# Kernel tuning notes

Measured on AMD Instinct MI355X. Metric: run time of the kernel, lower is better.

Reference implementation:

```python
import jax, jax.numpy as jnp
import numpy as np
import math

D_MODEL, N_HEADS, BATCH, SEQ = 1024, 16, 2, 2048
D_HEAD = D_MODEL // N_HEADS


def setup_inputs() -> dict:
    key = jax.random.key(0)
    ks = jax.random.split(key, 5)
    w = lambda k: jax.random.normal(k, (D_MODEL, D_MODEL), jnp.float32) * 0.02
    return {
        "X": jax.random.normal(ks[0], (BATCH, SEQ, D_MODEL), jnp.float32),
        "W_q": w(ks[1]),
        "W_k": w(ks[2]),
        "W_v": w(ks[3]),
        "W_o": w(ks[4]),
        "g_q": jnp.ones((D_MODEL,), jnp.float32),
        "b_q": jnp.zeros((D_MODEL,), jnp.float32),
        "g_k": jnp.ones((D_MODEL,), jnp.float32),
        "b_k": jnp.zeros((D_MODEL,), jnp.float32),
        "cache_k": jnp.zeros((BATCH, N_HEADS, SEQ, D_HEAD), jnp.float32),
        "cache_v": jnp.zeros((BATCH, N_HEADS, SEQ, D_HEAD), jnp.float32),
        "start_pos": 0,
    }


def _layernorm(x, g, b, eps=1e-5):
    mu = jnp.mean(x, axis=-1, keepdims=True)
    xc = x - mu
    var = jnp.mean(xc * xc, axis=-1, keepdims=True)
    return xc * jax.lax.rsqrt(var + eps) * g + b


def reference(X, W_q, W_k, W_v, W_o, g_q, b_q, g_k, b_k, cache_k, cache_v, start_pos):
    batch, N, d_model = X.shape
    H = cache_k.shape[1]
    dh = d_model // H

    # QK-normed projections (torch Linear: x @ W^T)
    XQ = _layernorm(X @ W_q.T, g_q, b_q)
    XK = _layernorm(X @ W_k.T, g_k, b_k)
    XV = X @ W_v.T
    split = lambda t: t.reshape(batch, N, H, dh).transpose(0, 2, 1, 3)  # [b,h,n,d]
    XQ, XK, XV = split(XQ), split(XK), split(XV)

    # KV-cache scatter update, then slice to valid prefix (start_pos is static)
    cache_k = jax.lax.dynamic_update_slice(cache_k, XK, (0, 0, start_pos, 0))
    cache_v = jax.lax.dynamic_update_slice(cache_v, XV, (0, 0, start_pos, 0))
    M = start_pos + N
    K = cache_k[:, :, :M]
    V = cache_v[:, :, :M]

    logits = jnp.einsum('bhnd,bhmd->bhnm', XQ, K) / math.sqrt(dh)  # [b,h,N,M]

    # causal mask on the freshly written block [start_pos:M]
    tril = jnp.tril(jnp.ones((N, N), bool))
    full_mask = jnp.concatenate([jnp.ones((N, start_pos), bool), tril], axis=1)  # [N,M]
    logits = jnp.where(full_mask[None, None], logits, -jnp.inf)

    # selective forget-mask bias built from relu'd head-0 logits
    S = jax.nn.relu(logits[:, 0])               # relu(-inf) -> 0, matches torch
    S = S.at[..., 0].set(0.0)                   # zero first column
    S = S * (1.0 - jnp.eye(N, dtype=S.dtype))   # zero diagonal (valid since start_pos==0)
    S = jnp.roll(S, 1, axis=-2)                 # shift rows down by one
    S = S.at[..., 0, :].set(0.0)
    F_mask = jnp.cumsum(S, axis=-2)             # [b,N,M]

    logits = logits - F_mask[:, None]
    attn = jax.nn.softmax(logits, axis=-1)
    O = jnp.einsum('bhnm,bhmd->bhnd', attn, V)
    O = O.transpose(0, 2, 1, 3).reshape(batch, N, d_model)
    return O @ W_o.T
```

## Files before the change

kernel.cpp:

```cpp
#include <hip/hip_runtime.h>
#include <cstdint>
#include <cstddef>


typedef unsigned short u16;
typedef __attribute__((ext_vector_type(8))) __bf16 bf16x8;
typedef __attribute__((ext_vector_type(4))) float f32x4;

#define D_MODEL 1024
#define N_HEADS 16
#define BATCH   2
#define SEQ     2048
#define D_HEAD  64
#define ROWS    (BATCH*SEQ)
#define NSEG    16
#define SEGLEN  128
#define LOG2E   1.44269504f

static __device__ __forceinline__ u16 f2bf(float f){
  union { float f; uint32_t u; } v; v.f = f;
  uint32_t r = v.u + 0x7fffu + ((v.u >> 16) & 1u);
  return (u16)(r >> 16);
}
static __device__ __forceinline__ float bf2f(u16 h){
  union { uint32_t u; float f; } v; v.u = ((uint32_t)h) << 16;
  return v.f;
}
static __device__ __forceinline__ uint32_t pack2(float a, float b){
  uint32_t ua = __float_as_uint(a) + 0x8000u;
  uint32_t ub = __float_as_uint(b) + 0x8000u;
  return (ua >> 16) | (ub & 0xffff0000u);
}

__global__ void k_cast_split_all(const float* __restrict__ X,
                                 u16* __restrict__ Xhi, u16* __restrict__ Xlo,
                                 const float* __restrict__ Wq,
                                 u16* __restrict__ Wqh, u16* __restrict__ Wql,
                                 const float* __restrict__ Wk,
                                 u16* __restrict__ Wkh, u16* __restrict__ Wkl){
  int i = blockIdx.x*256 + threadIdx.x;
  const float* src; u16 *dh, *dl; int base;
  if (i < 1048576){ src = X;  dh = Xhi; dl = Xlo; base = i; }
  else if (i < 1310720){ src = Wq; dh = Wqh; dl = Wql; base = i - 1048576; }
  else { src = Wk; dh = Wkh; dl = Wkl; base = i - 1310720; }
  float4 v = reinterpret_cast<const float4*>(src)[base];
  float vs[4] = {v.x, v.y, v.z, v.w};
  union { u16 s[4]; uint2 u; } uh, ul;
#pragma unroll
  for (int r=0;r<4;++r){
    uh.s[r] = f2bf(vs[r]);
    ul.s[r] = f2bf(vs[r] - bf2f(uh.s[r]));
  }
  reinterpret_cast<uint2*>(dh)[base] = uh.u;
  reinterpret_cast<uint2*>(dl)[base] = ul.u;
}

__global__ void k_cast2(const float* __restrict__ Wv, u16* __restrict__ Wvb,
                        const float* __restrict__ Wo, u16* __restrict__ Wob){
  int i = blockIdx.x*256 + threadIdx.x;
  const float* src; u16* dst; int base;
  if (i < 262144){ src = Wv; dst = Wvb; base = i; }
  else { src = Wo; dst = Wob; base = i - 262144; }
  float4 v = reinterpret_cast<const float4*>(src)[base];
  float vs[4] = {v.x, v.y, v.z, v.w};
  union { u16 s[4]; uint2 u; } uh;
#pragma unroll
  for (int r=0;r<4;++r) uh.s[r] = f2bf(vs[r]);
  reinterpret_cast<uint2*>(dst)[base] = uh.u;
}

__global__ __launch_bounds__(256) void k_gemm_qk(
    const u16* __restrict__ Xhi, const u16* __restrict__ Xlo,
    const u16* __restrict__ Wh, const u16* __restrict__ Wl,
    float* __restrict__ C)
{
  __shared__ __align__(16) u16 As[128*32];
  __shared__ __align__(16) u16 Bs[128*32];
  const int tid = threadIdx.x, wv = tid>>6, ln = tid&63;
  const int lane15 = ln&15, quad = ln>>4;
  const int wm = wv&1, wn = wv>>1;
  const size_t rowBase = (size_t)blockIdx.y*128, colBase = (size_t)blockIdx.x*128;
  const int npass = ((blockIdx.x & 7) == 0) ? 3 : 1;
  f32x4 acc[4][4];
  f32x4 z = {0.f,0.f,0.f,0.f};
#pragma unroll
  for (int i=0;i<4;++i)
#pragma unroll
    for (int j=0;j<4;++j) acc[i][j] = z;
  const u16* Aps[3] = {Xhi, Xhi, Xlo};
  const u16* Bps[3] = {Wh, Wl, Wh};
  const int sRow = ln>>2, sCol = (ln&3)*8;
  for (int p = 0; p < npass; ++p) {
    const u16* Ap = Aps[p];
    const u16* Bp = Bps[p];
    for (int kt = 0; kt < 32; ++kt) {
      __syncthreads();
#pragma unroll
      for (int c = 0; c < 2; ++c) {
        int chunk = wv*2 + c;
        int r = chunk*16 + sRow;
        const u16* ga = Ap + (rowBase + r)*1024 + kt*32 + sCol;
        const u16* gb = Bp + (colBase + r)*1024 + kt*32 + sCol;
        __builtin_amdgcn_global_load_lds(
            (const __attribute__((address_space(1))) void*)ga,
            (__attribute__((address_space(3))) void*)(As + chunk*512), 16, 0, 0);
        __builtin_amdgcn_global_load_lds(
            (const __attribute__((address_space(1))) void*)gb,
            (__attribute__((address_space(3))) void*)(Bs + chunk*512), 16, 0, 0);
      }
      __syncthreads();
      bf16x8 af[4], bfb[4];
#pragma unroll
      for (int t=0;t<4;++t){
        af[t]  = *reinterpret_cast<const bf16x8*>(As + (wm*64 + t*16 + lane15)*32 + quad*8);
        bfb[t] = *reinterpret_cast<const bf16x8*>(Bs + (wn*64 + t*16 + lane15)*32 + quad*8);
      }
#pragma unroll
      for (int i=0;i<4;++i)
#pragma unroll
        for (int j=0;j<4;++j)
          acc[i][j] = __builtin_amdgcn_mfma_f32_16x16x32_bf16(af[i], bfb[j], acc[i][j], 0,0,0);
    }
  }
#pragma unroll
  for (int i=0;i<4;++i){
    size_t row = rowBase + wm*64 + i*16 + quad*4;
#pragma unroll
    for (int j=0;j<4;++j){
      size_t col = colBase + wn*64 + j*16 + lane15;
#pragma unroll
      for (int r=0;r<4;++r)
        C[(row+r)*2048 + col] = acc[i][j][r];
    }
  }
}

__global__ __launch_bounds__(256) void k_ln_pack2(
    const float* __restrict__ C,
    const float* __restrict__ gq, const float* __restrict__ bq,
    const float* __restrict__ gk, const float* __restrict__ bk,
    u16* __restrict__ Qh, u16* __restrict__ Kh,
    u16* __restrict__ Q0l, u16* __restrict__ K0l)
{
  const int row = blockIdx.x;
  const int tid = threadIdx.x;
  const float* cr = C + (size_t)row*2048;
  float4 vq = reinterpret_cast<const float4*>(cr)[tid];
  float4 vk = reinterpret_cast<const float4*>(cr)[256 + tid];
  float sq  = vq.x+vq.y+vq.z+vq.w;
  float s2q = vq.x*vq.x+vq.y*vq.y+vq.z*vq.z+vq.w*vq.w;
  float sk  = vk.x+vk.y+vk.z+vk.w;
  float s2k = vk.x*vk.x+vk.y*vk.y+vk.z*vk.z+vk.w*vk.w;
#pragma unroll
  for (int o=32;o;o>>=1){
    sq += __shfl_xor(sq,o);  s2q += __shfl_xor(s2q,o);
    sk += __shfl_xor(sk,o);  s2k += __shfl_xor(s2k,o);
  }
  __shared__ float red[4][4];
  if ((tid&63)==0){
    red[tid>>6][0]=sq; red[tid>>6][1]=s2q; red[tid>>6][2]=sk; red[tid>>6][3]=s2k;
  }
  __syncthreads();
  sq  = red[0][0]+red[1][0]+red[2][0]+red[3][0];
  s2q = red[0][1]+red[1][1]+red[2][1]+red[3][1];
  sk  = red[0][2]+red[1][2]+red[2][2]+red[3][2];
  s2k = red[0][3]+red[1][3]+red[2][3]+red[3][3];
  const float muq = sq*(1.f/D_MODEL);
  const float rsq = rsqrtf(s2q*(1.f/D_MODEL) - muq*muq + 1e-5f);
  const float muk = sk*(1.f/D_MODEL);
  const float rsk = rsqrtf(s2k*(1.f/D_MODEL) - muk*muk + 1e-5f);
  const int b = row >> 11, n = row & (SEQ-1);
  const int h = tid >> 4, d0 = (tid & 15)*4;
  float4 gqv = reinterpret_cast<const float4*>(gq)[tid];
  float4 bqv = reinterpret_cast<const float4*>(bq)[tid];
  float4 gkv = reinterpret_cast<const float4*>(gk)[tid];
  float4 bkv = reinterpret_cast<const float4*>(bk)[tid];
  float xq[4] = {vq.x,vq.y,vq.z,vq.w}, xk[4] = {vk.x,vk.y,vk.z,vk.w};
  float gQ[4] = {gqv.x,gqv.y,gqv.z,gqv.w}, bQ[4] = {bqv.x,bqv.y,bqv.z,bqv.w};
  float gK[4] = {gkv.x,gkv.y,gkv.z,gkv.w}, bK[4] = {bkv.x,bkv.y,bkv.z,bkv.w};
  union { u16 s[4]; uint2 u; } qh, ql, kh, kl;
#pragma unroll
  for (int r=0;r<4;++r){
    float yq = (xq[r]-muq)*rsq*gQ[r] + bQ[r];
    qh.s[r] = f2bf(yq);
    ql.s[r] = f2bf(yq - bf2f(qh.s[r]));
    float yk = (xk[r]-muk)*rsk*gK[r] + bK[r];
    kh.s[r] = f2bf(yk);
    kl.s[r] = f2bf(yk - bf2f(kh.s[r]));
  }
  size_t dst = (((size_t)(b*N_HEADS + h))*SEQ + n)*D_HEAD + d0;
  *reinterpret_cast<uint2*>(Qh + dst) = qh.u;
  *reinterpret_cast<uint2*>(Kh + dst) = kh.u;
  if (h == 0){
    size_t dl = ((size_t)b*SEQ + n)*D_HEAD + d0;
    *reinterpret_cast<uint2*>(Q0l + dl) = ql.u;
    *reinterpret_cast<uint2*>(K0l + dl) = kl.u;
  }
}

__global__ __launch_bounds__(256) void k_gemm_vt(
    const u16* __restrict__ A0, const u16* __restrict__ B0,
    u16* __restrict__ Vt)
{
  __shared__ __align__(16) u16 smem[64*136];
  u16* As = smem;
  u16* Bs = smem + 128*32;
  const int tid = threadIdx.x, wv = tid>>6, ln = tid&63;
  const int lane15 = ln&15, quad = ln>>4;
  const int wm = wv&1, wn = wv>>1;
  const size_t rowBase = (size_t)blockIdx.y*128, colBase = (size_t)blockIdx.x*64;
  f32x4 acc[4][2];
  f32x4 z = {0.f,0.f,0.f,0.f};
#pragma unroll
  for (int i=0;i<4;++i){ acc[i][0] = z; acc[i][1] = z; }
  const int sRow = ln>>2, sCol = (ln&3)*8;
  for (int kt = 0; kt < 32; ++kt) {
    __syncthreads();
#pragma unroll
    for (int c = 0; c < 2; ++c) {
      int chunk = wv*2 + c;
      int r = chunk*16 + sRow;
      const u16* ga = A0 + (rowBase + r)*1024 + kt*32 + sCol;
      __builtin_amdgcn_global_load_lds(
          (const __attribute__((address_space(1))) void*)ga,
          (__attribute__((address_space(3))) void*)(As + chunk*512), 16, 0, 0);
    }
    {
      int r = wv*16 + sRow;
      const u16* gb = B0 + (colBase + r)*1024 + kt*32 + sCol;
      __builtin_amdgcn_global_load_lds(
          (const __attribute__((address_space(1))) void*)gb,
          (__attribute__((address_space(3))) void*)(Bs + wv*512), 16, 0, 0);
    }
    __syncthreads();
    bf16x8 af[4], bfb[2];
#pragma unroll
    for (int t=0;t<4;++t)
      af[t]  = *reinterpret_cast<const bf16x8*>(As + (wm*64 + t*16 + lane15)*32 + quad*8);
#pragma unroll
    for (int t=0;t<2;++t)
      bfb[t] = *reinterpret_cast<const bf16x8*>(Bs + (wn*32 + t*16 + lane15)*32 + quad*8);
#pragma unroll
    for (int i=0;i<4;++i)
#pragma unroll
      for (int j=0;j<2;++j)
        acc[i][j] = __builtin_amdgcn_mfma_f32_16x16x32_bf16(af[i], bfb[j], acc[i][j], 0,0,0);
  }
  __syncthreads();
#pragma unroll
  for (int i=0;i<4;++i){
    int nl = wm*64 + i*16 + quad*4;
#pragma unroll
    for (int j=0;j<2;++j){
      int dl = wn*32 + j*16 + lane15;
#pragma unroll
      for (int r=0;r<4;++r)
        smem[dl*136 + nl + r] = f2bf(acc[i][j][r]);
    }
  }
  __syncthreads();
  const int b = (int)blockIdx.y >> 4;
  const int n0 = ((int)blockIdx.y & 15) * 128;
  const int bh = b*N_HEADS + (int)blockIdx.x;
  const int d = tid >> 2, seg = tid & 3;
  u16* dst = Vt + ((size_t)(bh*64 + d))*SEQ + n0 + seg*32;
  const u16* srcl = smem + d*136 + seg*32;
#pragma unroll
  for (int k=0;k<4;++k)
    *reinterpret_cast<uint4*>(dst + k*8) = *reinterpret_cast<const uint4*>(srcl + k*8);
}

__global__ __launch_bounds__(256) void k_s0(
    const u16* Qh, const u16* Q0l, const u16* Kh, const u16* K0l,
    float* __restrict__ S0, float* __restrict__ seg)
{
  const int b = blockIdx.z;
  const int bm = blockIdx.y;
  const int bn = blockIdx.x;
  const int tid = threadIdx.x;
  if (bn > bm){
    if (tid < 128) seg[((size_t)b*NSEG + bm)*SEQ + bn*128 + tid] = 0.f;
    return;
  }
  float* Sb = S0 + (size_t)b*SEQ*SEQ;
  __shared__ __align__(16) u16 As[128*32];
  __shared__ __align__(16) u16 Bs[128*32];
  __shared__ float cs[2][128];
  const int wv = tid>>6, ln = tid&63;
  const int lane15 = ln&15, quad = ln>>4;
  const int wm = wv&1, wn = wv>>1;
  f32x4 acc[4][4];
  f32x4 z = {0.f,0.f,0.f,0.f};
#pragma unroll
  for (int i=0;i<4;++i)
#pragma unroll
    for (int j=0;j<4;++j) acc[i][j] = z;
  const u16* Qb  = Qh  + (size_t)b*N_HEADS*SEQ*D_HEAD;
  const u16* Kb  = Kh  + (size_t)b*N_HEADS*SEQ*D_HEAD;
  const u16* Qlb = Q0l + (size_t)b*SEQ*D_HEAD;
  const u16* Klb = K0l + (size_t)b*SEQ*D_HEAD;
  const u16* Aps[3] = {Qb, Qb, Qlb};
  const u16* Bps[3] = {Kb, Klb, Kb};
  const int sRow = ln>>2, sCol = (ln&3)*8;
  const size_t rowBase = (size_t)bm*128, colBase = (size_t)bn*128;
  for (int p = 0; p < 3; ++p) {
    const u16* Ap = Aps[p];
    const u16* Bp = Bps[p];
    for (int kt = 0; kt < 2; ++kt) {
      __syncthreads();
#pragma unroll
      for (int c = 0; c < 2; ++c) {
        int chunk = wv*2 + c;
        int r = chunk*16 + sRow;
        const u16* ga = Ap + (rowBase + r)*D_HEAD + kt*32 + sCol;
        const u16* gb = Bp + (colBase + r)*D_HEAD + kt*32 + sCol;
        __builtin_amdgcn_global_load_lds(
            (const __attribute__((address_space(1))) void*)ga,
            (__attribute__((address_space(3))) void*)(As + chunk*512), 16, 0, 0);
        __builtin_amdgcn_global_load_lds(
            (const __attribute__((address_space(1))) void*)gb,
            (__attribute__((address_space(3))) void*)(Bs + chunk*512), 16, 0, 0);
      }
      __syncthreads();
      bf16x8 af[4], bfb[4];
#pragma unroll
      for (int t=0;t<4;++t){
        af[t]  = *reinterpret_cast<const bf16x8*>(As + (wm*64 + t*16 + lane15)*32 + quad*8);
        bfb[t] = *reinterpret_cast<const bf16x8*>(Bs + (wn*64 + t*16 + lane15)*32 + quad*8);
      }
#pragma unroll
      for (int i=0;i<4;++i)
#pragma unroll
        for (int j=0;j<4;++j)
          acc[i][j] = __builtin_amdgcn_mfma_f32_16x16x32_bf16(af[i], bfb[j], acc[i][j], 0,0,0);
    }
  }
  float csum[4] = {0.f,0.f,0.f,0.f};
#pragma unroll
  for (int i=0;i<4;++i){
#pragma unroll
    for (int j=0;j<4;++j){
#pragma unroll
      for (int r=0;r<4;++r){
        int jg = (int)rowBase + wm*64 + i*16 + quad*4 + r;
        int mg = (int)colBase + wn*64 + j*16 + lane15;
        float l = acc[i][j][r]*0.125f;
        float s = (mg >= 1 && mg < jg) ? fmaxf(l, 0.f) : 0.f;
        Sb[(size_t)jg*SEQ + mg] = s;
        csum[j] += s;
      }
    }
  }
#pragma unroll
  for (int j=0;j<4;++j){
    float v = csum[j];
    v += __shfl_xor(v, 16);
    v += __shfl_xor(v, 32);
    if (ln < 16) cs[wm][wn*64 + j*16 + ln] = v;
  }
  __syncthreads();
  if (tid < 128)
    seg[((size_t)b*NSEG + bm)*SEQ + bn*128 + tid] = cs[0][tid] + cs[1][tid];
}

__global__ void k_seg_scan(float* __restrict__ seg){
  int m = blockIdx.x*256 + threadIdx.x;
  int b = blockIdx.y;
  float run = 0.f;
#pragma unroll
  for (int s=0;s<NSEG;++s){
    size_t idx = ((size_t)b*NSEG + s)*SEQ + m;
    float t = seg[idx]; seg[idx] = run; run += t;
  }
}
__global__ void k_seg_apply(float* __restrict__ SF, const float* __restrict__ seg){
  int m = blockIdx.x*256 + threadIdx.x;
  int s = blockIdx.y, b = blockIdx.z;
  float run = seg[((size_t)b*NSEG + s)*SEQ + m];
  float* Sb = SF + (size_t)b*SEQ*SEQ;
  const int j0 = s*SEGLEN;
  for (int i=0;i<SEGLEN;++i){
    size_t idx = (size_t)(j0 + i)*SEQ + m;
    float t = Sb[idx];
    Sb[idx] = -run*LOG2E;
    run += (j0 + i > m) ? t : 0.f;
  }
}

__global__ __launch_bounds__(256, 4) void k_attn(
    const u16* __restrict__ Qh, const u16* __restrict__ Kh,
    const u16* __restrict__ Vt, const float* __restrict__ F,
    u16* __restrict__ Ob)
{
  __shared__ __align__(16) u16 Ks[2][64*64];
  __shared__ __align__(16) u16 Vs[2][64*64];
  const int h = blockIdx.x, b = blockIdx.z;
  const int nt = b ? (int)(gridDim.y - 1 - blockIdx.y) : (int)blockIdx.y;
  const int tid = threadIdx.x, wv = tid>>6, ln = tid&63;
  const int lane15 = ln&15, quad = ln>>4;
  const u16* Qbh = Qh + ((size_t)(b*N_HEADS + h))*SEQ*D_HEAD;
  const u16* Kbh = Kh + ((size_t)(b*N_HEADS + h))*SEQ*D_HEAD;
  const u16* Vbh = Vt + ((size_t)(b*N_HEADS + h))*D_HEAD*SEQ;
  const float* Fb = F + (size_t)b*SEQ*SEQ;
  const int n_loc = wv*16 + lane15;
  const int n_g = nt*64 + n_loc;
  const int swz = (ln&7) ^ ((ln>>3)&7);
  const int fswz = lane15 & 7;
  const int srow = ln>>3;

  bf16x8 qf[2];
#pragma unroll
  for (int kt=0; kt<2; ++kt)
    qf[kt] = *reinterpret_cast<const bf16x8*>(Qbh + (size_t)n_g*D_HEAD + kt*32 + quad*8);

  f32x4 z = {0.f,0.f,0.f,0.f};
  f32x4 psum = z;
  f32x4 acc_o[4];
#pragma unroll
  for (int no=0;no<4;++no) acc_o[no] = z;

  auto stage = [&](int mt, int buf){
#pragma unroll
    for (int c=0;c<2;++c){
      int chunk = wv*2 + c;
      int r = chunk*8 + srow;
      const u16* gk = Kbh + (size_t)(mt*64 + r)*D_HEAD + swz*8;
      const u16* gv = Vbh + (size_t)r*SEQ + mt*64 + swz*8;
      __builtin_amdgcn_global_load_lds(
          (const __attribute__((address_space(1))) void*)gk,
          (__attribute__((address_space(3))) void*)(&Ks[buf][chunk*512]), 16, 0, 0);
      __builtin_amdgcn_global_load_lds(
          (const __attribute__((address_space(1))) void*)gv,
          (__attribute__((address_space(3))) void*)(&Vs[buf][chunk*512]), 16, 0, 0);
    }
  };
  stage(0, 0);
  const float c1 = 0.125f*LOG2E;

  for (int mt = 0; mt <= nt; ++mt) {
    const int cur = mt & 1;
    __syncthreads();
    if (mt < nt) stage(mt+1, 1-cur);
    const float* Fr = Fb + (size_t)n_g*SEQ + mt*64;
    f32x4 fv[4];
#pragma unroll
    for (int ms=0; ms<4; ++ms)
      fv[ms] = *reinterpret_cast<const f32x4*>(Fr + ms*16 + quad*4);
    f32x4 accs[4];
#pragma unroll
    for (int ms=0;ms<4;++ms) accs[ms] = z;
#pragma unroll
    for (int kt=0; kt<2; ++kt){
#pragma unroll
      for (int ms=0; ms<4; ++ms){
        bf16x8 a = *reinterpret_cast<const bf16x8*>(
            &Ks[cur][(ms*16 + lane15)*64 + (((kt*4 + quad) ^ fswz) * 8)]);
        accs[ms] = __builtin_amdgcn_mfma_f32_16x16x32_bf16(a, qf[kt], accs[ms], 0,0,0);
      }
    }
    const bool diag = (mt == nt);
    uint32_t pw[4][2];
#pragma unroll
    for (int ms=0; ms<4; ++ms){
      f32x4 t = accs[ms];
      float p[4];
#pragma unroll
      for (int r=0;r<4;++r){
        float l2 = fmaf(t[r], c1, fv[ms][r]);
        if (diag){
          int ml = ms*16 + quad*4 + r;
          l2 = (ml > n_loc) ? -1e30f : l2;
        }
        p[r] = __builtin_amdgcn_exp2f(l2);
      }
      psum[0]+=p[0]; psum[1]+=p[1]; psum[2]+=p[2]; psum[3]+=p[3];
      pw[ms][0] = pack2(p[0], p[1]);
      pw[ms][1] = pack2(p[2], p[3]);
    }
#pragma unroll
    for (int kt=0; kt<2; ++kt){
      union { uint32_t u[4]; bf16x8 v; } pa;
#pragma unroll
      for (int w=0; w<4; ++w){
        int sl = lane15 + 16*((quad&1)*2 + (w>>1));
        uint32_t t0 = (uint32_t)__shfl((int)pw[2*kt  ][w&1], sl);
        uint32_t t1 = (uint32_t)__shfl((int)pw[2*kt+1][w&1], sl);
        pa.u[w] = (quad < 2) ? t0 : t1;
      }
#pragma unroll
      for (int no=0; no<4; ++no){
        int d = no*16 + lane15;
        bf16x8 vb = *reinterpret_cast<const bf16x8*>(
            &Vs[cur][d*64 + (((kt*4 + quad) ^ (d&7)) * 8)]);
        acc_o[no] = __builtin_amdgcn_mfma_f32_16x16x32_bf16(pa.v, vb, acc_o[no], 0,0,0);
      }
    }
  }
  float s = (psum[0]+psum[1]) + (psum[2]+psum[3]);
  s += __shfl_xor(s, 16);
  s += __shfl_xor(s, 32);
  f32x4 inv;
#pragma unroll
  for (int r=0;r<4;++r)
    inv[r] = __builtin_amdgcn_rcpf(__shfl(s, quad*4 + r));
#pragma unroll
  for (int no=0; no<4; ++no){
#pragma unroll
    for (int r=0;r<4;++r){
      float o = acc_o[no][r] * inv[r];
      int row = nt*64 + wv*16 + quad*4 + r;
      Ob[((size_t)(b*SEQ + row))*D_MODEL + h*64 + no*16 + lane15] = f2bf(o);
    }
  }
}

__global__ __launch_bounds__(256) void k_gemm_nt64(
    const u16* __restrict__ A0, const u16* __restrict__ B0,
    float* __restrict__ C, int N, int K)
{
  __shared__ __align__(16) u16 As[128*32];
  __shared__ __align__(16) u16 Bs[64*32];
  const int tid = threadIdx.x, wv = tid>>6, ln = tid&63;
  const int lane15 = ln&15, quad = ln>>4;
  const int wm = wv&1, wn = wv>>1;
  const size_t rowBase = (size_t)blockIdx.y*128, colBase = (size_t)blockIdx.x*64;
  f32x4 acc[4][2];
  f32x4 z = {0.f,0.f,0.f,0.f};
#pragma unroll
  for (int i=0;i<4;++i){ acc[i][0] = z; acc[i][1] = z; }
  const int ktiles = K >> 5;
  const int sRow = ln>>2, sCol = (ln&3)*8;
  for (int kt = 0; kt < ktiles; ++kt) {
    __syncthreads();
#pragma unroll
    for (int c = 0; c < 2; ++c) {
      int chunk = wv*2 + c;
      int r = chunk*16 + sRow;
      const u16* ga = A0 + (rowBase + r)*K + kt*32 + sCol;
      __builtin_amdgcn_global_load_lds(
          (const __attribute__((address_space(1))) void*)ga,
          (__attribute__((address_space(3))) void*)(As + chunk*512), 16, 0, 0);
    }
    {
      int r = wv*16 + sRow;
      const u16* gb = B0 + (colBase + r)*K + kt*32 + sCol;
      __builtin_amdgcn_global_load_lds(
          (const __attribute__((address_space(1))) void*)gb,
          (__attribute__((address_space(3))) void*)(Bs + wv*512), 16, 0, 0);
    }
    __syncthreads();
    bf16x8 af[4], bfb[2];
#pragma unroll
    for (int t=0;t<4;++t)
      af[t]  = *reinterpret_cast<const bf16x8*>(As + (wm*64 + t*16 + lane15)*32 + quad*8);
#pragma unroll
    for (int t=0;t<2;++t)
      bfb[t] = *reinterpret_cast<const bf16x8*>(Bs + (wn*32 + t*16 + lane15)*32 + quad*8);
#pragma unroll
    for (int i=0;i<4;++i)
#pragma unroll
      for (int j=0;j<2;++j)
        acc[i][j] = __builtin_amdgcn_mfma_f32_16x16x32_bf16(af[i], bfb[j], acc[i][j], 0,0,0);
  }
#pragma unroll
  for (int i=0;i<4;++i){
    size_t row = rowBase + wm*64 + i*16 + quad*4;
#pragma unroll
    for (int j=0;j<2;++j){
      size_t col = colBase + wn*32 + j*16 + lane15;
#pragma unroll
      for (int r=0;r<4;++r)
        C[(row+r)*N + col] = acc[i][j][r];
    }
  }
}

extern "C" void kernel_launch(void* const* d_in, const int* in_sizes, int n_in,
                              void* d_out, int out_size, void* d_ws, size_t ws_size,
                              hipStream_t stream)
{
  (void)in_sizes; (void)n_in; (void)out_size; (void)ws_size;
  const float* X  = (const float*)d_in[0];
  const float* Wq = (const float*)d_in[1];
  const float* Wk = (const float*)d_in[2];
  const float* Wv = (const float*)d_in[3];
  const float* Wo = (const float*)d_in[4];
  const float* gq = (const float*)d_in[5];
  const float* bq = (const float*)d_in[6];
  const float* gk = (const float*)d_in[7];
  const float* bk = (const float*)d_in[8];
  float* out = (float*)d_out;

  char* ws = (char*)d_ws;
  size_t off = 0;
  auto alloc = [&](size_t bytes)->char*{
    char* p = ws + off; off += (bytes + 255) & ~(size_t)255; return p;
  };
  u16* Xhi  = (u16*)alloc((size_t)ROWS*D_MODEL*2);
  u16* Xlo  = (u16*)alloc((size_t)ROWS*D_MODEL*2);
  u16* Wqkh = (u16*)alloc((size_t)2*D_MODEL*D_MODEL*2);
  u16* Wqkl = (u16*)alloc((size_t)2*D_MODEL*D_MODEL*2);
  u16* Wvb  = (u16*)alloc((size_t)D_MODEL*D_MODEL*2);
  u16* Wob  = (u16*)alloc((size_t)D_MODEL*D_MODEL*2);
  u16* Qhp  = (u16*)alloc((size_t)BATCH*N_HEADS*SEQ*D_HEAD*2);
  u16* Khp  = (u16*)alloc((size_t)BATCH*N_HEADS*SEQ*D_HEAD*2);
  u16* Q0l  = (u16*)alloc((size_t)BATCH*SEQ*D_HEAD*2);
  u16* K0l  = (u16*)alloc((size_t)BATCH*SEQ*D_HEAD*2);
  u16* Vtp  = (u16*)alloc((size_t)BATCH*N_HEADS*D_HEAD*SEQ*2);
  u16* Obf  = (u16*)alloc((size_t)ROWS*D_MODEL*2);
  float* Seg = (float*)alloc((size_t)BATCH*NSEG*SEQ*4);
  float* SF  = (float*)alloc((size_t)BATCH*SEQ*SEQ*4);
  float* C32 = SF;

  k_cast_split_all<<<6144, 256, 0, stream>>>(
      X, Xhi, Xlo,
      Wq, Wqkh, Wqkl,
      Wk, Wqkh + (size_t)D_MODEL*D_MODEL, Wqkl + (size_t)D_MODEL*D_MODEL);
  k_cast2<<<2048, 256, 0, stream>>>(Wv, Wvb, Wo, Wob);

  k_gemm_qk<<<dim3(16, 32), 256, 0, stream>>>(Xhi, Xlo, Wqkh, Wqkl, C32);
  k_ln_pack2<<<ROWS, 256, 0, stream>>>(C32, gq, bq, gk, bk, Qhp, Khp, Q0l, K0l);
  k_gemm_vt<<<dim3(16, 32), 256, 0, stream>>>(Xhi, Wvb, Vtp);
  k_s0<<<dim3(16, 16, BATCH), 256, 0, stream>>>(Qhp, Q0l, Khp, K0l, SF, Seg);
  k_seg_scan<<<dim3(8, BATCH), 256, 0, stream>>>(Seg);
  k_seg_apply<<<dim3(8, NSEG, BATCH), 256, 0, stream>>>(SF, Seg);
  k_attn<<<dim3(N_HEADS, SEQ/64, BATCH), 256, 0, stream>>>(Qhp, Khp, Vtp, SF, Obf);
  k_gemm_nt64<<<dim3(16, 32), 256, 0, stream>>>(Obf, Wob, out, D_MODEL, D_MODEL);
}
```

Before: 331.4 us.

## Split head-0 split-precision correction passes into separate atomic GEMM and fold segment scan

The QK GEMM kernel previously ran three bf16 passes (hi*hi, hi*lo, lo*hi) only for the column blocks holding head 0. That made those blocks three times longer than the rest and left a load-imbalanced tail. Now every block does a single pass, and a new k_corr kernel computes the two correction terms as separate z-slices, adding them into C with atomicAdd. The separate segment-scan launch is also removed: each seg_apply block now sums the preceding segment totals itself. This trades an extra launch plus atomics, and some redundant prefix summing, for better balance and one fewer kernel.

```diff
diff --git a/kernel.cpp b/kernel.cpp
--- a/kernel.cpp
+++ b/kernel.cpp
@@ -70,8 +70,7 @@
 }
 
 __global__ __launch_bounds__(256) void k_gemm_qk(
-    const u16* __restrict__ Xhi, const u16* __restrict__ Xlo,
-    const u16* __restrict__ Wh, const u16* __restrict__ Wl,
+    const u16* __restrict__ A0, const u16* __restrict__ B0,
     float* __restrict__ C)
 {
   __shared__ __align__(16) u16 As[128*32];
@@ -80,47 +79,40 @@
   const int lane15 = ln&15, quad = ln>>4;
   const int wm = wv&1, wn = wv>>1;
   const size_t rowBase = (size_t)blockIdx.y*128, colBase = (size_t)blockIdx.x*128;
-  const int npass = ((blockIdx.x & 7) == 0) ? 3 : 1;
   f32x4 acc[4][4];
   f32x4 z = {0.f,0.f,0.f,0.f};
 #pragma unroll
   for (int i=0;i<4;++i)
 #pragma unroll
     for (int j=0;j<4;++j) acc[i][j] = z;
-  const u16* Aps[3] = {Xhi, Xhi, Xlo};
-  const u16* Bps[3] = {Wh, Wl, Wh};
   const int sRow = ln>>2, sCol = (ln&3)*8;
-  for (int p = 0; p < npass; ++p) {
-    const u16* Ap = Aps[p];
-    const u16* Bp = Bps[p];
-    for (int kt = 0; kt < 32; ++kt) {
-      __syncthreads();
-#pragma unroll
-      for (int c = 0; c < 2; ++c) {
-        int chunk = wv*2 + c;
-        int r = chunk*16 + sRow;
-        const u16* ga = Ap + (rowBase + r)*1024 + kt*32 + sCol;
-        const u16* gb = Bp + (colBase + r)*1024 + kt*32 + sCol;
-        __builtin_amdgcn_global_load_lds(
-            (const __attribute__((address_space(1))) void*)ga,
-            (__attribute__((address_space(3))) void*)(As + chunk*512), 16, 0, 0);
-        __builtin_amdgcn_global_load_lds(
-            (const __attribute__((address_space(1))) void*)gb,
-            (__attribute__((address_space(3))) void*)(Bs + chunk*512), 16, 0, 0);
-      }
-      __syncthreads();
-      bf16x8 af[4], bfb[4];
-#pragma unroll
-      for (int t=0;t<4;++t){
-        af[t]  = *reinterpret_cast<const bf16x8*>(As + (wm*64 + t*16 + lane15)*32 + quad*8);
-        bfb[t] = *reinterpret_cast<const bf16x8*>(Bs + (wn*64 + t*16 + lane15)*32 + quad*8);
-      }
-#pragma unroll
-      for (int i=0;i<4;++i)
-#pragma unroll
-        for (int j=0;j<4;++j)
-          acc[i][j] = __builtin_amdgcn_mfma_f32_16x16x32_bf16(af[i], bfb[j], acc[i][j], 0,0,0);
-    }
+  for (int kt = 0; kt < 32; ++kt) {
+    __syncthreads();
+#pragma unroll
+    for (int c = 0; c < 2; ++c) {
+      int chunk = wv*2 + c;
+      int r = chunk*16 + sRow;
+      const u16* ga = A0 + (rowBase + r)*1024 + kt*32 + sCol;
+      const u16* gb = B0 + (colBase + r)*1024 + kt*32 + sCol;
+      __builtin_amdgcn_global_load_lds(
+          (const __attribute__((address_space(1))) void*)ga,
+          (__attribute__((address_space(3))) void*)(As + chunk*512), 16, 0, 0);
+      __builtin_amdgcn_global_load_lds(
+          (const __attribute__((address_space(1))) void*)gb,
+          (__attribute__((address_space(3))) void*)(Bs + chunk*512), 16, 0, 0);
+    }
+    __syncthreads();
+    bf16x8 af[4], bfb[4];
+#pragma unroll
+    for (int t=0;t<4;++t){
+      af[t]  = *reinterpret_cast<const bf16x8*>(As + (wm*64 + t*16 + lane15)*32 + quad*8);
+      bfb[t] = *reinterpret_cast<const bf16x8*>(Bs + (wn*64 + t*16 + lane15)*32 + quad*8);
+    }
+#pragma unroll
+    for (int i=0;i<4;++i)
+#pragma unroll
+      for (int j=0;j<4;++j)
+        acc[i][j] = __builtin_amdgcn_mfma_f32_16x16x32_bf16(af[i], bfb[j], acc[i][j], 0,0,0);
   }
 #pragma unroll
   for (int i=0;i<4;++i){
@@ -131,6 +123,71 @@
 #pragma unroll
       for (int r=0;r<4;++r)
         C[(row+r)*2048 + col] = acc[i][j][r];
+    }
+  }
+}
+
+__global__ __launch_bounds__(256) void k_corr(
+    const u16* __restrict__ Xhi, const u16* __restrict__ Xlo,
+    const u16* __restrict__ Wh, const u16* __restrict__ Wl,
+    float* __restrict__ C)
+{
+  __shared__ __align__(16) u16 As[128*32];
+  __shared__ __align__(16) u16 Bs[64*32];
+  const int tid = threadIdx.x, wv = tid>>6, ln = tid&63;
+  const int lane15 = ln&15, quad = ln>>4;
+  const int wm = wv&1, wn = wv>>1;
+  const size_t rowBase = (size_t)blockIdx.y*128;
+  const size_t wbase = blockIdx.x ? (size_t)1024*1024 : 0;
+  const size_t cbase = blockIdx.x ? 1024 : 0;
+  const u16* Ap = blockIdx.z ? Xlo : Xhi;
+  const u16* Bp = (blockIdx.z ? Wh : Wl) + wbase;
+  f32x4 acc[4][2];
+  f32x4 z = {0.f,0.f,0.f,0.f};
+#pragma unroll
+  for (int i=0;i<4;++i){ acc[i][0] = z; acc[i][1] = z; }
+  const int sRow = ln>>2, sCol = (ln&3)*8;
+  for (int kt = 0; kt < 32; ++kt) {
+    __syncthreads();
+#pragma unroll
+    for (int c = 0; c < 2; ++c) {
+      int chunk = wv*2 + c;
+      int r = chunk*16 + sRow;
+      const u16* ga = Ap + (rowBase + r)*1024 + kt*32 + sCol;
+      __builtin_amdgcn_global_load_lds(
+          (const __attribute__((address_space(1))) void*)ga,
+          (__attribute__((address_space(3))) void*)(As + chunk*512), 16, 0, 0);
+    }
+    {
+      int r = wv*16 + sRow;
+      const u16* gb = Bp + (size_t)r*1024 + kt*32 + sCol;
+      __builtin_amdgcn_global_load_lds(
+          (const __attribute__((address_space(1))) void*)gb,
+          (__attribute__((address_space(3))) void*)(Bs + wv*512), 16, 0, 0);
+    }
+    __syncthreads();
+    bf16x8 af[4], bfb[2];
+#pragma unroll
+    for (int t=0;t<4;++t)
+      af[t]  = *reinterpret_cast<const bf16x8*>(As + (wm*64 + t*16 + lane15)*32 + quad*8);
+#pragma unroll
+    for (int t=0;t<2;++t)
+      bfb[t] = *reinterpret_cast<const bf16x8*>(Bs + (wn*32 + t*16 + lane15)*32 + quad*8);
+#pragma unroll
+    for (int i=0;i<4;++i)
+#pragma unroll
+      for (int j=0;j<2;++j)
+        acc[i][j] = __builtin_amdgcn_mfma_f32_16x16x32_bf16(af[i], bfb[j], acc[i][j], 0,0,0);
+  }
+#pragma unroll
+  for (int i=0;i<4;++i){
+    size_t row = rowBase + wm*64 + i*16 + quad*4;
+#pragma unroll
+    for (int j=0;j<2;++j){
+      size_t col = cbase + wn*32 + j*16 + lane15;
+#pragma unroll
+      for (int r=0;r<4;++r)
+        atomicAdd(&C[(row+r)*2048 + col], acc[i][j][r]);
     }
   }
 }
@@ -363,20 +420,12 @@
     seg[((size_t)b*NSEG + bm)*SEQ + bn*128 + tid] = cs[0][tid] + cs[1][tid];
 }
 
-__global__ void k_seg_scan(float* __restrict__ seg){
-  int m = blockIdx.x*256 + threadIdx.x;
-  int b = blockIdx.y;
-  float run = 0.f;
-#pragma unroll
-  for (int s=0;s<NSEG;++s){
-    size_t idx = ((size_t)b*NSEG + s)*SEQ + m;
-    float t = seg[idx]; seg[idx] = run; run += t;
-  }
-}
 __global__ void k_seg_apply(float* __restrict__ SF, const float* __restrict__ seg){
   int m = blockIdx.x*256 + threadIdx.x;
   int s = blockIdx.y, b = blockIdx.z;
-  float run = seg[((size_t)b*NSEG + s)*SEQ + m];
+  const float* sb = seg + (size_t)b*NSEG*SEQ;
+  float run = 0.f;
+  for (int t=0; t<s; ++t) run += sb[(size_t)t*SEQ + m];
   float* Sb = SF + (size_t)b*SEQ*SEQ;
   const int j0 = s*SEGLEN;
   for (int i=0;i<SEGLEN;++i){
@@ -618,11 +667,11 @@
       Wk, Wqkh + (size_t)D_MODEL*D_MODEL, Wqkl + (size_t)D_MODEL*D_MODEL);
   k_cast2<<<2048, 256, 0, stream>>>(Wv, Wvb, Wo, Wob);
 
-  k_gemm_qk<<<dim3(16, 32), 256, 0, stream>>>(Xhi, Xlo, Wqkh, Wqkl, C32);
+  k_gemm_qk<<<dim3(16, 32), 256, 0, stream>>>(Xhi, Wqkh, C32);
+  k_corr<<<dim3(2, 32, 2), 256, 0, stream>>>(Xhi, Xlo, Wqkh, Wqkl, C32);
   k_ln_pack2<<<ROWS, 256, 0, stream>>>(C32, gq, bq, gk, bk, Qhp, Khp, Q0l, K0l);
   k_gemm_vt<<<dim3(16, 32), 256, 0, stream>>>(Xhi, Wvb, Vtp);
   k_s0<<<dim3(16, 16, BATCH), 256, 0, stream>>>(Qhp, Q0l, Khp, K0l, SF, Seg);
-  k_seg_scan<<<dim3(8, BATCH), 256, 0, stream>>>(Seg);
   k_seg_apply<<<dim3(8, NSEG, BATCH), 256, 0, stream>>>(SF, Seg);
   k_attn<<<dim3(N_HEADS, SEQ/64, BATCH), 256, 0, stream>>>(Qhp, Khp, Vtp, SF, Obf);
   k_gemm_nt64<<<dim3(16, 32), 256, 0, stream>>>(Obf, Wob, out, D_MODEL, D_MODEL);
```

Measured after the change: 312.2 us. 1.06x faster.
